# Kernel optimization log

Measured on AMD Instinct MI355X. Metric: run time of the kernel, lower is better.

The kernel has to match this reference:

```python
import jax, jax.numpy as jnp
import numpy as np

N = 32768      # total nodes
E = 524288     # edges (avg degree 16)
HID = 256      # hidden_dim
H = 8          # heads
C = HID // H   # head dim = 32
G = 64         # graphs in batch
NPG = N // G   # nodes per graph = 512
EDIM = 2       # edge feature dim
NEG_SLOPE = 0.2  # PyG GATv2 default


def setup_inputs():
    key = jax.random.key(0)
    ks = jax.random.split(key, 12)
    s = 0.05
    return dict(
        x=jax.random.normal(ks[0], (N, HID), jnp.float32),
        edge_attr=jax.random.normal(ks[1], (E, EDIM), jnp.float32),
        # GATv2Conv params
        W_l=jax.random.normal(ks[2], (HID, HID), jnp.float32) * s,
        b_l=jnp.zeros((HID,), jnp.float32),
        W_r=jax.random.normal(ks[3], (HID, HID), jnp.float32) * s,
        b_r=jnp.zeros((HID,), jnp.float32),
        W_e=jax.random.normal(ks[4], (EDIM, HID), jnp.float32) * s,
        att=jax.random.normal(ks[5], (H, C), jnp.float32) * s,
        bias_gat=jnp.zeros((HID,), jnp.float32),
        # MultiheadAttention params (torch packed qkv layout)
        in_proj_w=jax.random.normal(ks[6], (3 * HID, HID), jnp.float32) * s,
        in_proj_b=jnp.zeros((3 * HID,), jnp.float32),
        out_proj_w=jax.random.normal(ks[7], (HID, HID), jnp.float32) * s,
        out_proj_b=jnp.zeros((HID,), jnp.float32),
        alpha_param=jnp.array(0.5, jnp.float32),
        # FFN
        W1=jax.random.normal(ks[8], (HID, 4 * HID), jnp.float32) * s,
        b1=jnp.zeros((4 * HID,), jnp.float32),
        W2=jax.random.normal(ks[9], (4 * HID, HID), jnp.float32) * s,
        b2=jnp.zeros((HID,), jnp.float32),
        # LayerNorms
        g1=jnp.ones((HID,), jnp.float32), be1=jnp.zeros((HID,), jnp.float32),
        g2=jnp.ones((HID,), jnp.float32), be2=jnp.zeros((HID,), jnp.float32),
        g3=jnp.ones((HID,), jnp.float32), be3=jnp.zeros((HID,), jnp.float32),
        edge_index=jax.random.randint(ks[10], (2, E), 0, N, jnp.int32),
        batch=jnp.repeat(jnp.arange(G, dtype=jnp.int32), NPG),
    )


def _ln(x, g, b, eps=1e-5):
    m = jnp.mean(x, -1, keepdims=True)
    v = jnp.mean((x - m) ** 2, -1, keepdims=True)
    return (x - m) * jax.lax.rsqrt(v + eps) * g + b


def _gatv2(x, edge_index, edge_attr, W_l, b_l, W_r, b_r, W_e, att, bias_gat):
    src, dst = edge_index[0], edge_index[1]
    # PyG add_self_loops with fill_value='mean': self-loop edge_attr at node i
    # is the mean of edge_attr over edges incoming to i (0 if none).
    deg = jax.ops.segment_sum(jnp.ones((E,), x.dtype), dst, num_segments=N)
    ea_mean = jax.ops.segment_sum(edge_attr, dst, num_segments=N) / jnp.maximum(deg, 1.0)[:, None]
    loop = jnp.arange(N, dtype=src.dtype)
    src2 = jnp.concatenate([src, loop])
    dst2 = jnp.concatenate([dst, loop])
    ea2 = jnp.concatenate([edge_attr, ea_mean], axis=0)  # [E+N, 2]
    xl = (x @ W_l + b_l).reshape(N, H, C)  # source transform (messages)
    xr = (x @ W_r + b_r).reshape(N, H, C)  # target transform
    ee = (ea2 @ W_e).reshape(-1, H, C)
    e = jax.nn.leaky_relu(xl[src2] + xr[dst2] + ee, NEG_SLOPE)  # [E+N, H, C]
    score = jnp.einsum('ehc,hc->eh', e, att)  # [E+N, H]
    # scatter softmax over incoming edges of each target node
    smax = jax.lax.stop_gradient(jax.ops.segment_max(score, dst2, num_segments=N))
    ex = jnp.exp(score - smax[dst2])
    ssum = jax.ops.segment_sum(ex, dst2, num_segments=N)
    alpha = ex / ssum[dst2]  # [E+N, H]
    out = jax.ops.segment_sum(alpha[:, :, None] * xl[src2], dst2, num_segments=N)
    return out.reshape(N, HID) + bias_gat


def _mha(xg, in_proj_w, in_proj_b, out_proj_w, out_proj_b):
    # xg: [G, NPG, HID]; torch nn.MultiheadAttention (batch_first, eval mode)
    qkv = xg @ in_proj_w.T + in_proj_b
    q, k, v = jnp.split(qkv, 3, axis=-1)
    q = q.reshape(G, NPG, H, C)
    k = k.reshape(G, NPG, H, C)
    v = v.reshape(G, NPG, H, C)
    scores = jnp.einsum('gqhd,gkhd->ghqk', q, k) / jnp.sqrt(jnp.float32(C))
    p = jax.nn.softmax(scores, axis=-1)
    o = jnp.einsum('ghqk,gkhd->gqhd', p, v).reshape(G, NPG, HID)
    return o @ out_proj_w.T + out_proj_b


def reference(x, edge_attr, W_l, b_l, W_r, b_r, W_e, att, bias_gat,
              in_proj_w, in_proj_b, out_proj_w, out_proj_b, alpha_param,
              W1, b1, W2, b2, g1, be1, g2, be2, g3, be3, edge_index, batch):
    local_out = _ln(
        _gatv2(x, edge_index, edge_attr, W_l, b_l, W_r, b_r, W_e, att, bias_gat),
        g1, be1)
    # batch is sorted with equal-sized graphs -> the per-graph ragged
    # attention loop equals one batched [G, NPG, NPG] attention
    xg = x.reshape(G, NPG, HID)
    global_out = _mha(xg, in_proj_w, in_proj_b, out_proj_w, out_proj_b).reshape(N, HID)
    global_out = _ln(global_out, g2, be2)
    a = jax.nn.sigmoid(alpha_param)
    combined = a * local_out + (1.0 - a) * global_out
    ffn = jax.nn.gelu(combined @ W1 + b1, approximate=False) @ W2 + b2
    return _ln(combined + ffn, g3, be3)
```

## Files before the change

### kernel.cpp

```cpp
#include <hip/hip_runtime.h>
#include <math.h>

#define N_NODES 32768
#define E_EDGES 524288
#define HIDDEN  256
#define NPG     512
#define NGRAPH  64
#define NHEAD   8
#define CDIM    32

typedef unsigned short bf16;
typedef __attribute__((ext_vector_type(8))) short short8;
typedef __attribute__((ext_vector_type(4))) float f4;

#define AS1 __attribute__((address_space(1)))
#define AS3 __attribute__((address_space(3)))

__device__ __forceinline__ void cp16(const bf16* g, bf16* l) {
    __builtin_amdgcn_global_load_lds((AS1 const unsigned int*)(const void*)g,
                                     (AS3 unsigned int*)(void*)l, 16, 0, 0);
}

__device__ inline float bf2f(unsigned short u) {
    union { unsigned int i; float f; } v; v.i = ((unsigned int)u) << 16; return v.f;
}
__device__ inline unsigned short f2bf(float f) {
    union { float f; unsigned int i; } v; v.f = f;
    unsigned int x = v.i;
    return (unsigned short)((x + 0x7FFFu + ((x >> 16) & 1u)) >> 16);
}
__device__ inline float4 load4(const float* p) { return *(const float4*)p; }
__device__ inline float4 load4(const bf16* p) {
    ushort4 u = *(const ushort4*)p;
    return make_float4(bf2f(u.x), bf2f(u.y), bf2f(u.z), bf2f(u.w));
}
__device__ inline void store4(float* p, float4 v) { *(float4*)p = v; }
__device__ inline void store4(bf16* p, float4 v) {
    ushort4 u; u.x = f2bf(v.x); u.y = f2bf(v.y); u.z = f2bf(v.z); u.w = f2bf(v.w);
    *(ushort4*)p = u;
}


__global__ void zero_kernel(float* deg, float* ea_sum, int* fill) {
    int i = blockIdx.x * blockDim.x + threadIdx.x;
    if (i < 2 * N_NODES) ea_sum[i] = 0.0f;
    if (i < N_NODES) { deg[i] = 0.0f; fill[i] = 0; }
}

__global__ void deg_kernel(const int* __restrict__ ei, const float* __restrict__ edge_attr,
                           float* deg, float* ea_sum) {
    int e = blockIdx.x * blockDim.x + threadIdx.x;
    if (e >= E_EDGES) return;
    int d = ei[E_EDGES + e];
    atomicAdd(&deg[d], 1.0f);
    atomicAdd(&ea_sum[2 * d + 0], edge_attr[2 * e + 0]);
    atomicAdd(&ea_sum[2 * d + 1], edge_attr[2 * e + 1]);
}

__global__ void eamean_kernel(const float* __restrict__ deg, float* ea_mean) {
    int i = blockIdx.x * blockDim.x + threadIdx.x;
    if (i >= N_NODES) return;
    float dm = fmaxf(deg[i], 1.0f);
    ea_mean[2 * i + 0] /= dm;
    ea_mean[2 * i + 1] /= dm;
}

__global__ __launch_bounds__(1024) void scan_kernel(const float* __restrict__ deg, int* row_ptr) {
    __shared__ int part[1024];
    int t = threadIdx.x;
    int base = t * 32;
    int loc[32];
    int s = 0;
    #pragma unroll
    for (int j = 0; j < 32; j++) {
        loc[j] = s;
        s += (int)deg[base + j] + 1;
    }
    int mysum = s;
    part[t] = s;
    __syncthreads();
    for (int off = 1; off < 1024; off <<= 1) {
        int v = 0;
        if (t >= off) v = part[t - off];
        __syncthreads();
        part[t] += v;
        __syncthreads();
    }
    int offset = part[t] - mysum;
    #pragma unroll
    for (int j = 0; j < 32; j++) row_ptr[base + j] = offset + loc[j];
    if (t == 1023) row_ptr[N_NODES] = part[1023];
}

__global__ void fill_kernel(const int* __restrict__ ei, const int* __restrict__ row_ptr,
                            int* fill, int* col) {
    int tid = blockIdx.x * blockDim.x + threadIdx.x;
    if (tid >= E_EDGES + N_NODES) return;
    int d;
    if (tid < E_EDGES) d = ei[E_EDGES + tid];
    else               d = tid - E_EDGES;
    int pos = row_ptr[d] + atomicAdd(&fill[d], 1);
    col[pos] = tid;
}

__global__ void convall(const float* __restrict__ x,
                        const float* __restrict__ W_l, const float* __restrict__ W_r,
                        const float* __restrict__ W1, const float* __restrict__ W2,
                        const float* __restrict__ in_proj_w, const float* __restrict__ out_proj_w,
                        const float* __restrict__ b_l, const float* __restrict__ b_r,
                        bf16* xb, bf16* wlrb, bf16* w1b, bf16* w2b,
                        bf16* wipb, bf16* wopb, float* blr)
{
    int b = blockIdx.x, t = threadIdx.x;
    if (b < 8192) {
        int i = b * 256 + t;
        store4(&xb[i * 4], *(const float4*)&x[i * 4]);
    } else if (b < 8448) {
        int i = (b - 8192) * 256 + t; int k = i >> 8, n = i & 255;
        wlrb[n * 256 + k] = f2bf(W_l[i]);
    } else if (b < 8704) {
        int i = (b - 8448) * 256 + t; int k = i >> 8, n = i & 255;
        wlrb[(256 + n) * 256 + k] = f2bf(W_r[i]);
    } else if (b < 9728) {
        int i = (b - 8704) * 256 + t; int k = i >> 10, n = i & 1023;
        w1b[n * 256 + k] = f2bf(W1[i]);
    } else if (b < 10752) {
        int i = (b - 9728) * 256 + t; int k = i >> 8, n = i & 255;
        w2b[n * 1024 + k] = f2bf(W2[i]);
    } else if (b < 10944) {
        int i = (b - 10752) * 256 + t;
        store4(&wipb[i * 4], *(const float4*)&in_proj_w[i * 4]);
    } else if (b < 11008) {
        int i = (b - 10944) * 256 + t;
        store4(&wopb[i * 4], *(const float4*)&out_proj_w[i * 4]);
    } else {
        blr[t] = b_l[t]; blr[256 + t] = b_r[t];
    }
}

template <int EPI>
__global__ __launch_bounds__(256) void mfma_gemm(
    const bf16* __restrict__ A, const bf16* __restrict__ Wb,
    const float* __restrict__ bias, const bf16* __restrict__ res,
    bf16* __restrict__ C, int M, int N, int K)
{
    __shared__ bf16 lds[2 * 128 * 64];
    bf16* As = lds;
    bf16* Bs = lds + 128 * 64;
    int tid = threadIdx.x;
    int wave = tid >> 6, lane = tid & 63;
    int quad = lane >> 4, l16 = lane & 15;
    int n0 = blockIdx.x * 128, m0 = blockIdx.y * 128;
    int wm = (wave & 1) * 64, wn = (wave >> 1) * 64;

    f4 acc[4][4] = {};

    int srow = tid >> 3;
    int scol = (tid & 7) * 8;

    for (int k0 = 0; k0 < K; k0 += 64) {
        #pragma unroll
        for (int i = 0; i < 4; i++) {
            int row = i * 32 + srow;
            cp16(&A[(size_t)(m0 + row) * K + k0 + scol], &As[row * 64 + scol]);
            cp16(&Wb[(size_t)(n0 + row) * K + k0 + scol], &Bs[row * 64 + scol]);
        }
        __syncthreads();
        #pragma unroll
        for (int ks = 0; ks < 2; ks++) {
            short8 af[4], bfr[4];
            #pragma unroll
            for (int mt = 0; mt < 4; mt++)
                af[mt] = *(const short8*)&As[(wm + mt * 16 + l16) * 64 + ks * 32 + quad * 8];
            #pragma unroll
            for (int nt = 0; nt < 4; nt++)
                bfr[nt] = *(const short8*)&Bs[(wn + nt * 16 + l16) * 64 + ks * 32 + quad * 8];
            #pragma unroll
            for (int mt = 0; mt < 4; mt++)
                #pragma unroll
                for (int nt = 0; nt < 4; nt++)
                    acc[mt][nt] = __builtin_amdgcn_mfma_f32_16x16x32_bf16(
                        af[mt], bfr[nt], acc[mt][nt], 0, 0, 0);
        }
        __syncthreads();
    }

    float* epi = (float*)lds + wave * 16 * 68;
    int row = lane >> 2;
    int cb = (lane & 3) * 16;
    int gn = n0 + wn + cb;
    float bb[16];
    *(float4*)&bb[0]  = *(const float4*)&bias[gn + 0];
    *(float4*)&bb[4]  = *(const float4*)&bias[gn + 4];
    *(float4*)&bb[8]  = *(const float4*)&bias[gn + 8];
    *(float4*)&bb[12] = *(const float4*)&bias[gn + 12];

    for (int mt = 0; mt < 4; mt++) {
        #pragma unroll
        for (int nt = 0; nt < 4; nt++)
            #pragma unroll
            for (int r = 0; r < 4; r++)
                epi[(quad * 4 + r) * 68 + nt * 16 + l16] = acc[mt][nt][r];
        float vv[16];
        *(float4*)&vv[0]  = *(float4*)&epi[row * 68 + cb + 0];
        *(float4*)&vv[4]  = *(float4*)&epi[row * 68 + cb + 4];
        *(float4*)&vv[8]  = *(float4*)&epi[row * 68 + cb + 8];
        *(float4*)&vv[12] = *(float4*)&epi[row * 68 + cb + 12];
        int gm = m0 + wm + mt * 16 + row;
        #pragma unroll
        for (int j = 0; j < 16; j++) vv[j] += bb[j];
        if (EPI == 1) {
            #pragma unroll
            for (int j = 0; j < 16; j++)
                vv[j] = 0.5f * vv[j] * (1.0f + erff(vv[j] * 0.70710678118654752f));
        } else if (EPI == 2) {
            ushort rr[16];
            const bf16* rp = &res[(size_t)gm * N + gn];
            *(int4*)&rr[0] = *(const int4*)&rp[0];
            *(int4*)&rr[8] = *(const int4*)&rp[8];
            #pragma unroll
            for (int j = 0; j < 16; j++) vv[j] += bf2f(rr[j]);
        }
        ushort o16[16];
        #pragma unroll
        for (int j = 0; j < 16; j++) o16[j] = f2bf(vv[j]);
        bf16* cp = &C[(size_t)gm * N + gn];
        *(int4*)&cp[0] = *(int4*)&o16[0];
        *(int4*)&cp[8] = *(int4*)&o16[8];
    }
}

__global__ __launch_bounds__(256) void attn_mfma(
    const bf16* __restrict__ qkv, bf16* __restrict__ attnout)
{
    __shared__ bf16 Ks[128 * 40];
    __shared__ bf16 Vt[32 * 136];
    __shared__ bf16 Pb[4 * 64 * 40];

    int b = blockIdx.x;
    int g = b >> 4, h = (b >> 1) & 7, hlf = b & 1;
    int tid = threadIdx.x;
    int wave = tid >> 6, lane = tid & 63;
    int quad = lane >> 4, l16 = lane & 15;
    int qbase = hlf * 256 + wave * 64;
    bf16* Pw = &Pb[wave * 64 * 40];
    const float SCALE = 0.17677669529663687f;

    short8 qf[4];
    #pragma unroll
    for (int mt = 0; mt < 4; mt++) {
        size_t node = (size_t)(g * NPG + qbase + mt * 16 + l16);
        qf[mt] = *(const short8*)&qkv[node * 768 + h * CDIM + quad * 8];
    }

    f4 oacc[4][2] = {};
    float lacc[4][4] = {};

    for (int c = 0; c < 4; c++) {
        int kk0 = c * 128;
        __syncthreads();
        #pragma unroll
        for (int i = 0; i < 2; i++) {
            int idx = i * 256 + tid;
            int key = idx >> 2, kc = (idx & 3) * 8;
            *(int4*)&Ks[key * 40 + kc] =
                *(const int4*)&qkv[(size_t)(g * NPG + kk0 + key) * 768 + 256 + h * CDIM + kc];
        }
        {
            int key = tid >> 1, dblk = (tid & 1) * 16;
            ushort tmp[16];
            const bf16* vp = &qkv[(size_t)(g * NPG + kk0 + key) * 768 + 512 + h * CDIM + dblk];
            *(int4*)&tmp[0] = *(const int4*)&vp[0];
            *(int4*)&tmp[8] = *(const int4*)&vp[8];
            #pragma unroll
            for (int j = 0; j < 16; j++) Vt[(dblk + j) * 136 + key] = tmp[j];
        }
        __syncthreads();

        for (int sub = 0; sub < 4; sub++) {
            int ks0 = sub * 32;
            short8 kf[2];
            #pragma unroll
            for (int nt = 0; nt < 2; nt++)
                kf[nt] = *(const short8*)&Ks[(ks0 + nt * 16 + l16) * 40 + quad * 8];
            #pragma unroll
            for (int mt = 0; mt < 4; mt++) {
                #pragma unroll
                for (int nt = 0; nt < 2; nt++) {
                    f4 z = {0.f, 0.f, 0.f, 0.f};
                    f4 s = __builtin_amdgcn_mfma_f32_16x16x32_bf16(qf[mt], kf[nt], z, 0, 0, 0);
                    #pragma unroll
                    for (int r = 0; r < 4; r++) {
                        float p = __expf(s[r] * SCALE);
                        lacc[mt][r] += p;
                        Pw[(mt * 16 + quad * 4 + r) * 40 + nt * 16 + l16] = f2bf(p);
                    }
                }
            }
            short8 vf[2];
            #pragma unroll
            for (int dt = 0; dt < 2; dt++)
                vf[dt] = *(const short8*)&Vt[(dt * 16 + l16) * 136 + ks0 + quad * 8];
            #pragma unroll
            for (int mt = 0; mt < 4; mt++) {
                short8 pf = *(const short8*)&Pw[(mt * 16 + l16) * 40 + quad * 8];
                #pragma unroll
                for (int dt = 0; dt < 2; dt++)
                    oacc[mt][dt] = __builtin_amdgcn_mfma_f32_16x16x32_bf16(
                        pf, vf[dt], oacc[mt][dt], 0, 0, 0);
            }
        }
    }

    #pragma unroll
    for (int mt = 0; mt < 4; mt++)
        #pragma unroll
        for (int r = 0; r < 4; r++) {
            float l = lacc[mt][r];
            l += __shfl_xor(l, 1);
            l += __shfl_xor(l, 2);
            l += __shfl_xor(l, 4);
            l += __shfl_xor(l, 8);
            lacc[mt][r] = l;
        }

    #pragma unroll
    for (int mt = 0; mt < 4; mt++) {
        #pragma unroll
        for (int dt = 0; dt < 2; dt++) {
            #pragma unroll
            for (int r = 0; r < 4; r++) {
                float v = oacc[mt][dt][r] / lacc[mt][r];
                size_t node = (size_t)(g * NPG + qbase + mt * 16 + quad * 4 + r);
                attnout[node * HIDDEN + h * CDIM + dt * 16 + l16] = f2bf(v);
            }
        }
    }
}

__device__ __forceinline__ void fetchmeta(
    int i, int re, int node, const int* __restrict__ col, const int* __restrict__ ei,
    const float* __restrict__ edge_attr, const float* __restrict__ ea_mean,
    int& s, float& a0, float& a1)
{
    if (i < re) {
        int e = col[i];
        if (e < E_EDGES) {
            s = ei[e]; a0 = edge_attr[2 * e]; a1 = edge_attr[2 * e + 1];
        } else {
            s = node; a0 = ea_mean[2 * node]; a1 = ea_mean[2 * node + 1];
        }
    } else {
        s = node; a0 = 0.f; a1 = 0.f;
    }
}

__global__ __launch_bounds__(256) void gat_kernel(
    const bf16* __restrict__ xlr,
    const int* __restrict__ row_ptr, const int* __restrict__ col,
    const int* __restrict__ ei, const float* __restrict__ edge_attr,
    const float* __restrict__ ea_mean,
    const float* __restrict__ W_e, const float* __restrict__ att,
    const float* __restrict__ bias_gat,
    const float* __restrict__ g1, const float* __restrict__ be1,
    bf16* __restrict__ out)
{
    __shared__ float pacc[2][260];
    __shared__ float plsum[2][64];
    int wave = threadIdx.x >> 6;
    int lane = threadIdx.x & 63;
    int nloc = wave >> 1, half = wave & 1;
    int node = blockIdx.x * 2 + nloc;
    int cb = lane * 4;

    float4 xr4 = load4(&xlr[(size_t)node * 512 + 256 + cb]);
    float4 we0 = *(const float4*)&W_e[cb];
    float4 we1 = *(const float4*)&W_e[HIDDEN + cb];
    float4 at4 = *(const float4*)&att[cb];

    int rs = row_ptr[node], re = row_ptr[node + 1];

    float lsum = 0.f;
    float acc0 = 0.f, acc1 = 0.f, acc2 = 0.f, acc3 = 0.f;

    int i0 = rs + half;
    int s0, s1; float a00, a01, a10, a11;
    fetchmeta(i0,     re, node, col, ei, edge_attr, ea_mean, s0, a00, a01);
    fetchmeta(i0 + 2, re, node, col, ei, edge_attr, ea_mean, s1, a10, a11);
    ushort4 xu0 = *(const ushort4*)&xlr[(size_t)s0 * 512 + cb];

    for (int i = i0; i < re; i += 2) {
        int s2; float a20, a21;
        fetchmeta(i + 4, re, node, col, ei, edge_attr, ea_mean, s2, a20, a21);
        ushort4 xu1 = *(const ushort4*)&xlr[(size_t)s1 * 512 + cb];

        float4 xl4 = make_float4(bf2f(xu0.x), bf2f(xu0.y), bf2f(xu0.z), bf2f(xu0.w));
        float t, p = 0.f;
        t = xl4.x + xr4.x + a00 * we0.x + a01 * we1.x; t = (t > 0.f) ? t : 0.2f * t; p += t * at4.x;
        t = xl4.y + xr4.y + a00 * we0.y + a01 * we1.y; t = (t > 0.f) ? t : 0.2f * t; p += t * at4.y;
        t = xl4.z + xr4.z + a00 * we0.z + a01 * we1.z; t = (t > 0.f) ? t : 0.2f * t; p += t * at4.z;
        t = xl4.w + xr4.w + a00 * we0.w + a01 * we1.w; t = (t > 0.f) ? t : 0.2f * t; p += t * at4.w;
        p += __shfl_xor(p, 1);
        p += __shfl_xor(p, 2);
        p += __shfl_xor(p, 4);
        float w = __expf(p);
        lsum += w;
        acc0 += w * xl4.x; acc1 += w * xl4.y; acc2 += w * xl4.z; acc3 += w * xl4.w;

        s0 = s1; a00 = a10; a01 = a11; xu0 = xu1;
        s1 = s2; a10 = a20; a11 = a21;
    }

    if (half) {
        plsum[nloc][lane] = lsum;
        pacc[nloc][cb + 0] = acc0; pacc[nloc][cb + 1] = acc1;
        pacc[nloc][cb + 2] = acc2; pacc[nloc][cb + 3] = acc3;
    }
    __syncthreads();
    if (!half) {
        lsum += plsum[nloc][lane];
        acc0 += pacc[nloc][cb + 0]; acc1 += pacc[nloc][cb + 1];
        acc2 += pacc[nloc][cb + 2]; acc3 += pacc[nloc][cb + 3];

        float inv = 1.0f / lsum;
        float v0 = acc0 * inv + bias_gat[cb + 0];
        float v1 = acc1 * inv + bias_gat[cb + 1];
        float v2 = acc2 * inv + bias_gat[cb + 2];
        float v3 = acc3 * inv + bias_gat[cb + 3];

        float s = v0 + v1 + v2 + v3;
        #pragma unroll
        for (int m = 1; m < 64; m <<= 1) s += __shfl_xor(s, m);
        float mean = s * (1.0f / 256.0f);
        float d0 = v0 - mean, d1 = v1 - mean, d2 = v2 - mean, d3 = v3 - mean;
        float sq = d0 * d0 + d1 * d1 + d2 * d2 + d3 * d3;
        #pragma unroll
        for (int m = 1; m < 64; m <<= 1) sq += __shfl_xor(sq, m);
        float rstd = rsqrtf(sq * (1.0f / 256.0f) + 1e-5f);
        float4 o;
        o.x = d0 * rstd * g1[cb + 0] + be1[cb + 0];
        o.y = d1 * rstd * g1[cb + 1] + be1[cb + 1];
        o.z = d2 * rstd * g1[cb + 2] + be1[cb + 2];
        o.w = d3 * rstd * g1[cb + 3] + be1[cb + 3];
        store4(&out[(size_t)node * HIDDEN + cb], o);
    }
}

__global__ __launch_bounds__(256) void combine_kernel(
    const bf16* __restrict__ gout, const bf16* __restrict__ localout,
    const float* __restrict__ alpha_p,
    const float* __restrict__ g2, const float* __restrict__ be2,
    bf16* __restrict__ combined)
{
    int wave = threadIdx.x >> 6;
    int lane = threadIdx.x & 63;
    int node = blockIdx.x * 4 + wave;
    int cb = lane * 4;
    float4 gv = load4(&gout[(size_t)node * HIDDEN + cb]);
    float s = gv.x + gv.y + gv.z + gv.w;
    #pragma unroll
    for (int m = 1; m < 64; m <<= 1) s += __shfl_xor(s, m);
    float mean = s * (1.0f / 256.0f);
    float d0 = gv.x - mean, d1 = gv.y - mean, d2 = gv.z - mean, d3 = gv.w - mean;
    float sq = d0 * d0 + d1 * d1 + d2 * d2 + d3 * d3;
    #pragma unroll
    for (int m = 1; m < 64; m <<= 1) sq += __shfl_xor(sq, m);
    float rstd = rsqrtf(sq * (1.0f / 256.0f) + 1e-5f);
    float n0 = d0 * rstd * g2[cb + 0] + be2[cb + 0];
    float n1 = d1 * rstd * g2[cb + 1] + be2[cb + 1];
    float n2 = d2 * rstd * g2[cb + 2] + be2[cb + 2];
    float n3 = d3 * rstd * g2[cb + 3] + be2[cb + 3];
    float a = 1.0f / (1.0f + __expf(-alpha_p[0]));
    float4 lv = load4(&localout[(size_t)node * HIDDEN + cb]);
    float4 o;
    o.x = a * lv.x + (1.0f - a) * n0;
    o.y = a * lv.y + (1.0f - a) * n1;
    o.z = a * lv.z + (1.0f - a) * n2;
    o.w = a * lv.w + (1.0f - a) * n3;
    store4(&combined[(size_t)node * HIDDEN + cb], o);
}

__global__ __launch_bounds__(256) void finalln_kernel(
    const bf16* __restrict__ ffn,
    const float* __restrict__ g3, const float* __restrict__ be3,
    float* __restrict__ out)
{
    int wave = threadIdx.x >> 6;
    int lane = threadIdx.x & 63;
    int node = blockIdx.x * 4 + wave;
    int cb = lane * 4;
    float4 v = load4(&ffn[(size_t)node * HIDDEN + cb]);
    float s = v.x + v.y + v.z + v.w;
    #pragma unroll
    for (int m = 1; m < 64; m <<= 1) s += __shfl_xor(s, m);
    float mean = s * (1.0f / 256.0f);
    float d0 = v.x - mean, d1 = v.y - mean, d2 = v.z - mean, d3 = v.w - mean;
    float sq = d0 * d0 + d1 * d1 + d2 * d2 + d3 * d3;
    #pragma unroll
    for (int m = 1; m < 64; m <<= 1) sq += __shfl_xor(sq, m);
    float rstd = rsqrtf(sq * (1.0f / 256.0f) + 1e-5f);
    float4 o;
    o.x = d0 * rstd * g3[cb + 0] + be3[cb + 0];
    o.y = d1 * rstd * g3[cb + 1] + be3[cb + 1];
    o.z = d2 * rstd * g3[cb + 2] + be3[cb + 2];
    o.w = d3 * rstd * g3[cb + 3] + be3[cb + 3];
    *(float4*)&out[(size_t)node * HIDDEN + cb] = o;
}

extern "C" void kernel_launch(void* const* d_in, const int* in_sizes, int n_in,
                              void* d_out, int out_size, void* d_ws, size_t ws_size,
                              hipStream_t stream) {
    const float* x          = (const float*)d_in[0];
    const float* edge_attr  = (const float*)d_in[1];
    const float* W_l        = (const float*)d_in[2];
    const float* b_l        = (const float*)d_in[3];
    const float* W_r        = (const float*)d_in[4];
    const float* b_r        = (const float*)d_in[5];
    const float* W_e        = (const float*)d_in[6];
    const float* att        = (const float*)d_in[7];
    const float* bias_gat   = (const float*)d_in[8];
    const float* in_proj_w  = (const float*)d_in[9];
    const float* in_proj_b  = (const float*)d_in[10];
    const float* out_proj_w = (const float*)d_in[11];
    const float* out_proj_b = (const float*)d_in[12];
    const float* alpha_p    = (const float*)d_in[13];
    const float* W1         = (const float*)d_in[14];
    const float* b1         = (const float*)d_in[15];
    const float* W2         = (const float*)d_in[16];
    const float* b2         = (const float*)d_in[17];
    const float* g1  = (const float*)d_in[18];
    const float* be1 = (const float*)d_in[19];
    const float* g2  = (const float*)d_in[20];
    const float* be2 = (const float*)d_in[21];
    const float* g3  = (const float*)d_in[22];
    const float* be3 = (const float*)d_in[23];
    const int* edge_index = (const int*)d_in[24];

    char* base = (char*)d_ws;
    const size_t MB = 1024 * 1024;
    const size_t KB = 1024;
    float* deg     = (float*)(base + 0);
    float* ea_mean = (float*)(base + 131072);
    int*   fill    = (int*)  (base + 393216);
    int*   row_ptr = (int*)  (base + 524288);
    int*   col     = (int*)  (base + 786432);
    bf16* wlrb = (bf16*)(base + 3 * MB);
    bf16* wipb = (bf16*)(base + 3 * MB + 256 * KB);
    bf16* wopb = (bf16*)(base + 3 * MB + 640 * KB);
    bf16* w1b  = (bf16*)(base + 3 * MB + 768 * KB);
    bf16* w2b  = (bf16*)(base + 3 * MB + 1280 * KB);
    float* blr = (float*)(base + 5 * MB);
    bf16* xb       = (bf16*)(base + 8 * MB);
    bf16* qkv      = (bf16*)(base + 24 * MB);
    bf16* attnout  = (bf16*)(base + 72 * MB);
    bf16* gout     = (bf16*)(base + 24 * MB);
    bf16* xlr      = (bf16*)(base + 40 * MB);
    bf16* localout = (bf16*)(base + 72 * MB);
    bf16* combined = (bf16*)(base + 8 * MB);
    bf16* h1h      = (bf16*)(base + 24 * MB);
    bf16* ffn      = (bf16*)(base + 56 * MB);
    float* out = (float*)d_out;

    zero_kernel<<<(2 * N_NODES + 255) / 256, 256, 0, stream>>>(deg, ea_mean, fill);
    deg_kernel<<<E_EDGES / 256, 256, 0, stream>>>(edge_index, edge_attr, deg, ea_mean);
    eamean_kernel<<<N_NODES / 256, 256, 0, stream>>>(deg, ea_mean);
    scan_kernel<<<1, 1024, 0, stream>>>(deg, row_ptr);
    fill_kernel<<<(E_EDGES + N_NODES) / 256, 256, 0, stream>>>(edge_index, row_ptr, fill, col);

    convall<<<11009, 256, 0, stream>>>(x, W_l, W_r, W1, W2, in_proj_w, out_proj_w,
                                       b_l, b_r, xb, wlrb, w1b, w2b, wipb, wopb, blr);

    mfma_gemm<0><<<dim3(6, 256), 256, 0, stream>>>(
        xb, wipb, in_proj_b, (const bf16*)nullptr, qkv, N_NODES, 768, 256);
    attn_mfma<<<NGRAPH * NHEAD * 2, 256, 0, stream>>>(qkv, attnout);
    mfma_gemm<0><<<dim3(2, 256), 256, 0, stream>>>(
        attnout, wopb, out_proj_b, (const bf16*)nullptr, gout, N_NODES, 256, 256);

    mfma_gemm<0><<<dim3(4, 256), 256, 0, stream>>>(
        xb, wlrb, blr, (const bf16*)nullptr, xlr, N_NODES, 512, 256);
    gat_kernel<<<N_NODES / 2, 256, 0, stream>>>(
        xlr, row_ptr, col, edge_index, edge_attr, ea_mean,
        W_e, att, bias_gat, g1, be1, localout);

    combine_kernel<<<N_NODES / 4, 256, 0, stream>>>(
        gout, localout, alpha_p, g2, be2, combined);

    for (int hh = 0; hh < 2; hh++) {
        const bf16* ch = combined + (size_t)hh * 16384 * 256;
        bf16* fh = ffn + (size_t)hh * 16384 * 256;
        mfma_gemm<1><<<dim3(8, 128), 256, 0, stream>>>(
            ch, w1b, b1, (const bf16*)nullptr, h1h, 16384, 1024, 256);
        mfma_gemm<2><<<dim3(2, 128), 256, 0, stream>>>(
            h1h, w2b, b2, ch, fh, 16384, 256, 1024);
    }

    finalln_kernel<<<N_NODES / 4, 256, 0, stream>>>(ffn, g3, be3, out);
}
```

Baseline: 609.6 us.

## Split GAT xl/xr outputs into dense arrays and transpose attention score MFMA

The x_l/x_r projection GEMM gets a new epilogue that writes its two halves into separate 256-wide arrays, so the GAT gather reads dense 512-byte rows instead of strided halves of 1024-byte rows. In the attention kernel, V is now staged row-major with vector copies instead of a scalar transpose into shared memory. Scores are computed as K·Qᵀ so each lane packs four probabilities into one 8-byte store and accumulates row sums that need only two cross-lane shuffles. The cost is that V fragments are now gathered element by element from shared memory, and the row sums pass through an extra shared buffer.

Measured after the change: 616.3 us. About the same (+1.1%).

```diff
diff --git a/kernel.cpp b/kernel.cpp
--- a/kernel.cpp
+++ b/kernel.cpp
@@ -224,7 +224,14 @@
         ushort o16[16];
         #pragma unroll
         for (int j = 0; j < 16; j++) o16[j] = f2bf(vv[j]);
-        bf16* cp = &C[(size_t)gm * N + gn];
+        bf16* cp;
+        if (EPI == 3) {
+            bf16* dst = (gn < 256) ? C : (bf16*)res;
+            int goff = (gn < 256) ? gn : gn - 256;
+            cp = &dst[(size_t)gm * 256 + goff];
+        } else {
+            cp = &C[(size_t)gm * N + gn];
+        }
         *(int4*)&cp[0] = *(int4*)&o16[0];
         *(int4*)&cp[8] = *(int4*)&o16[8];
     }
@@ -234,8 +241,9 @@
     const bf16* __restrict__ qkv, bf16* __restrict__ attnout)
 {
     __shared__ bf16 Ks[128 * 40];
-    __shared__ bf16 Vt[32 * 136];
+    __shared__ bf16 Vs[128 * 40];
     __shared__ bf16 Pb[4 * 64 * 40];
+    __shared__ float lsumS[4][64];
 
     int b = blockIdx.x;
     int g = b >> 4, h = (b >> 1) & 7, hlf = b & 1;
@@ -248,13 +256,13 @@
 
     short8 qf[4];
     #pragma unroll
-    for (int mt = 0; mt < 4; mt++) {
-        size_t node = (size_t)(g * NPG + qbase + mt * 16 + l16);
-        qf[mt] = *(const short8*)&qkv[node * 768 + h * CDIM + quad * 8];
+    for (int qt = 0; qt < 4; qt++) {
+        size_t node = (size_t)(g * NPG + qbase + qt * 16 + l16);
+        qf[qt] = *(const short8*)&qkv[node * 768 + h * CDIM + quad * 8];
     }
 
     f4 oacc[4][2] = {};
-    float lacc[4][4] = {};
+    float ls[4] = {0.f, 0.f, 0.f, 0.f};
 
     for (int c = 0; c < 4; c++) {
         int kk0 = c * 128;
@@ -263,17 +271,9 @@
         for (int i = 0; i < 2; i++) {
             int idx = i * 256 + tid;
             int key = idx >> 2, kc = (idx & 3) * 8;
-            *(int4*)&Ks[key * 40 + kc] =
-                *(const int4*)&qkv[(size_t)(g * NPG + kk0 + key) * 768 + 256 + h * CDIM + kc];
-        }
-        {
-            int key = tid >> 1, dblk = (tid & 1) * 16;
-            ushort tmp[16];
-            const bf16* vp = &qkv[(size_t)(g * NPG + kk0 + key) * 768 + 512 + h * CDIM + dblk];
-            *(int4*)&tmp[0] = *(const int4*)&vp[0];
-            *(int4*)&tmp[8] = *(const int4*)&vp[8];
-            #pragma unroll
-            for (int j = 0; j < 16; j++) Vt[(dblk + j) * 136 + key] = tmp[j];
+            const bf16* bp = &qkv[(size_t)(g * NPG + kk0 + key) * 768 + h * CDIM + kc];
+            *(int4*)&Ks[key * 40 + kc] = *(const int4*)(bp + 256);
+            *(int4*)&Vs[key * 40 + kc] = *(const int4*)(bp + 512);
         }
         __syncthreads();
 
@@ -281,26 +281,35 @@
             int ks0 = sub * 32;
             short8 kf[2];
             #pragma unroll
-            for (int nt = 0; nt < 2; nt++)
-                kf[nt] = *(const short8*)&Ks[(ks0 + nt * 16 + l16) * 40 + quad * 8];
-            #pragma unroll
-            for (int mt = 0; mt < 4; mt++) {
+            for (int kt = 0; kt < 2; kt++)
+                kf[kt] = *(const short8*)&Ks[(ks0 + kt * 16 + l16) * 40 + quad * 8];
+            #pragma unroll
+            for (int kt = 0; kt < 2; kt++) {
                 #pragma unroll
-                for (int nt = 0; nt < 2; nt++) {
+                for (int qt = 0; qt < 4; qt++) {
                     f4 z = {0.f, 0.f, 0.f, 0.f};
-                    f4 s = __builtin_amdgcn_mfma_f32_16x16x32_bf16(qf[mt], kf[nt], z, 0, 0, 0);
+                    f4 st = __builtin_amdgcn_mfma_f32_16x16x32_bf16(kf[kt], qf[qt], z, 0, 0, 0);
+                    ushort pk[4];
+                    float s4 = 0.f;
                     #pragma unroll
                     for (int r = 0; r < 4; r++) {
-                        float p = __expf(s[r] * SCALE);
-                        lacc[mt][r] += p;
-                        Pw[(mt * 16 + quad * 4 + r) * 40 + nt * 16 + l16] = f2bf(p);
+                        float p = __expf(st[r] * SCALE);
+                        s4 += p;
+                        pk[r] = f2bf(p);
                     }
+                    ls[qt] += s4;
+                    *(uint2*)&Pw[(qt * 16 + l16) * 40 + kt * 16 + quad * 4] = *(uint2*)pk;
                 }
             }
             short8 vf[2];
             #pragma unroll
-            for (int dt = 0; dt < 2; dt++)
-                vf[dt] = *(const short8*)&Vt[(dt * 16 + l16) * 136 + ks0 + quad * 8];
+            for (int dt = 0; dt < 2; dt++) {
+                ushort vtmp[8];
+                #pragma unroll
+                for (int j = 0; j < 8; j++)
+                    vtmp[j] = Vs[(ks0 + quad * 8 + j) * 40 + dt * 16 + l16];
+                vf[dt] = *(short8*)vtmp;
+            }
             #pragma unroll
             for (int mt = 0; mt < 4; mt++) {
                 short8 pf = *(const short8*)&Pw[(mt * 16 + l16) * 40 + quad * 8];
@@ -313,16 +322,13 @@
     }
 
     #pragma unroll
-    for (int mt = 0; mt < 4; mt++)
-        #pragma unroll
-        for (int r = 0; r < 4; r++) {
-            float l = lacc[mt][r];
-            l += __shfl_xor(l, 1);
-            l += __shfl_xor(l, 2);
-            l += __shfl_xor(l, 4);
-            l += __shfl_xor(l, 8);
-            lacc[mt][r] = l;
-        }
+    for (int qt = 0; qt < 4; qt++) {
+        float l = ls[qt];
+        l += __shfl_xor(l, 16);
+        l += __shfl_xor(l, 32);
+        if (quad == 0) lsumS[wave][qt * 16 + l16] = l;
+    }
+    __builtin_amdgcn_s_waitcnt(0);
 
     #pragma unroll
     for (int mt = 0; mt < 4; mt++) {
@@ -330,7 +336,8 @@
         for (int dt = 0; dt < 2; dt++) {
             #pragma unroll
             for (int r = 0; r < 4; r++) {
-                float v = oacc[mt][dt][r] / lacc[mt][r];
+                float denom = lsumS[wave][mt * 16 + quad * 4 + r];
+                float v = oacc[mt][dt][r] / denom;
                 size_t node = (size_t)(g * NPG + qbase + mt * 16 + quad * 4 + r);
                 attnout[node * HIDDEN + h * CDIM + dt * 16 + l16] = f2bf(v);
             }
@@ -356,7 +363,7 @@
 }
 
 __global__ __launch_bounds__(256) void gat_kernel(
-    const bf16* __restrict__ xlr,
+    const bf16* __restrict__ xl, const bf16* __restrict__ xr,
     const int* __restrict__ row_ptr, const int* __restrict__ col,
     const int* __restrict__ ei, const float* __restrict__ edge_attr,
     const float* __restrict__ ea_mean,
@@ -373,7 +380,7 @@
     int node = blockIdx.x * 2 + nloc;
     int cb = lane * 4;
 
-    float4 xr4 = load4(&xlr[(size_t)node * 512 + 256 + cb]);
+    float4 xr4 = load4(&xr[(size_t)node * 256 + cb]);
     float4 we0 = *(const float4*)&W_e[cb];
     float4 we1 = *(const float4*)&W_e[HIDDEN + cb];
     float4 at4 = *(const float4*)&att[cb];
@@ -387,12 +394,12 @@
     int s0, s1; float a00, a01, a10, a11;
     fetchmeta(i0,     re, node, col, ei, edge_attr, ea_mean, s0, a00, a01);
     fetchmeta(i0 + 2, re, node, col, ei, edge_attr, ea_mean, s1, a10, a11);
-    ushort4 xu0 = *(const ushort4*)&xlr[(size_t)s0 * 512 + cb];
+    ushort4 xu0 = *(const ushort4*)&xl[(size_t)s0 * 256 + cb];
 
     for (int i = i0; i < re; i += 2) {
         int s2; float a20, a21;
         fetchmeta(i + 4, re, node, col, ei, edge_attr, ea_mean, s2, a20, a21);
-        ushort4 xu1 = *(const ushort4*)&xlr[(size_t)s1 * 512 + cb];
+        ushort4 xu1 = *(const ushort4*)&xl[(size_t)s1 * 256 + cb];
 
         float4 xl4 = make_float4(bf2f(xu0.x), bf2f(xu0.y), bf2f(xu0.z), bf2f(xu0.w));
         float t, p = 0.f;
@@ -554,7 +561,8 @@
     bf16* qkv      = (bf16*)(base + 24 * MB);
     bf16* attnout  = (bf16*)(base + 72 * MB);
     bf16* gout     = (bf16*)(base + 24 * MB);
-    bf16* xlr      = (bf16*)(base + 40 * MB);
+    bf16* xl       = (bf16*)(base + 40 * MB);
+    bf16* xr       = (bf16*)(base + 56 * MB);
     bf16* localout = (bf16*)(base + 72 * MB);
     bf16* combined = (bf16*)(base + 8 * MB);
     bf16* h1h      = (bf16*)(base + 24 * MB);
@@ -576,10 +584,10 @@
     mfma_gemm<0><<<dim3(2, 256), 256, 0, stream>>>(
         attnout, wopb, out_proj_b, (const bf16*)nullptr, gout, N_NODES, 256, 256);
 
-    mfma_gemm<0><<<dim3(4, 256), 256, 0, stream>>>(
-        xb, wlrb, blr, (const bf16*)nullptr, xlr, N_NODES, 512, 256);
+    mfma_gemm<3><<<dim3(4, 256), 256, 0, stream>>>(
+        xb, wlrb, blr, (const bf16*)xr, xl, N_NODES, 512, 256);
     gat_kernel<<<N_NODES / 2, 256, 0, stream>>>(
-        xlr, row_ptr, col, edge_index, edge_attr, ea_mean,
+        xl, xr, row_ptr, col, edge_index, edge_attr, ea_mean,
         W_e, att, bias_gat, g1, be1, localout);
 
     combine_kernel<<<N_NODES / 4, 256, 0, stream>>>(
```

## Pack CSR edge records and split xl/xr outputs for GAT gather

Applied to the files above, without the earlier changes.

The fill kernel now writes a packed 16-byte record per CSR slot holding the source node and both edge attributes. This replaces the col index that forced gat_kernel to make a dependent second gather into edge_index and edge_attr. The lin_l/lin_r GEMM gets a new epilogue (EPI 3) that writes xl and xr into two separate N x 256 arrays instead of one interleaved 512-wide buffer. Source-row gathers therefore hit a compact array with better cache density. The cost is a larger CSR buffer (16 bytes per edge instead of 4) plus extra reads in fill_kernel.

New measurement: 590.7 us. 3.1% less time.

```diff
diff --git a/kernel.cpp b/kernel.cpp
--- a/kernel.cpp
+++ b/kernel.cpp
@@ -92,15 +92,30 @@
     if (t == 1023) row_ptr[N_NODES] = part[1023];
 }
 
-__global__ void fill_kernel(const int* __restrict__ ei, const int* __restrict__ row_ptr,
-                            int* fill, int* col) {
+__global__ void fill_kernel(const int* __restrict__ ei, const float* __restrict__ edge_attr,
+                            const float* __restrict__ ea_mean,
+                            const int* __restrict__ row_ptr, int* fill, int4* __restrict__ erec) {
     int tid = blockIdx.x * blockDim.x + threadIdx.x;
     if (tid >= E_EDGES + N_NODES) return;
-    int d;
-    if (tid < E_EDGES) d = ei[E_EDGES + tid];
-    else               d = tid - E_EDGES;
+    int d, src; float a0, a1;
+    if (tid < E_EDGES) {
+        d = ei[E_EDGES + tid];
+        src = ei[tid];
+        a0 = edge_attr[2 * tid + 0];
+        a1 = edge_attr[2 * tid + 1];
+    } else {
+        d = tid - E_EDGES;
+        src = d;
+        a0 = ea_mean[2 * d + 0];
+        a1 = ea_mean[2 * d + 1];
+    }
     int pos = row_ptr[d] + atomicAdd(&fill[d], 1);
-    col[pos] = tid;
+    int4 r;
+    r.x = src;
+    r.y = __float_as_int(a0);
+    r.z = __float_as_int(a1);
+    r.w = 0;
+    erec[pos] = r;
 }
 
 __global__ void convall(const float* __restrict__ x,
@@ -224,7 +239,14 @@
         ushort o16[16];
         #pragma unroll
         for (int j = 0; j < 16; j++) o16[j] = f2bf(vv[j]);
-        bf16* cp = &C[(size_t)gm * N + gn];
+        bf16* cp;
+        if (EPI == 3) {
+            bf16* dst = (gn < 256) ? C : (bf16*)res;
+            int goff = (gn < 256) ? gn : gn - 256;
+            cp = &dst[(size_t)gm * 256 + goff];
+        } else {
+            cp = &C[(size_t)gm * N + gn];
+        }
         *(int4*)&cp[0] = *(int4*)&o16[0];
         *(int4*)&cp[8] = *(int4*)&o16[8];
     }
@@ -338,28 +360,21 @@
     }
 }
 
-__device__ __forceinline__ void fetchmeta(
-    int i, int re, int node, const int* __restrict__ col, const int* __restrict__ ei,
-    const float* __restrict__ edge_attr, const float* __restrict__ ea_mean,
+__device__ __forceinline__ void fetchrec(
+    int i, int re, int node, const int4* __restrict__ erec,
     int& s, float& a0, float& a1)
 {
     if (i < re) {
-        int e = col[i];
-        if (e < E_EDGES) {
-            s = ei[e]; a0 = edge_attr[2 * e]; a1 = edge_attr[2 * e + 1];
-        } else {
-            s = node; a0 = ea_mean[2 * node]; a1 = ea_mean[2 * node + 1];
-        }
+        int4 r = erec[i];
+        s = r.x; a0 = __int_as_float(r.y); a1 = __int_as_float(r.z);
     } else {
         s = node; a0 = 0.f; a1 = 0.f;
     }
 }
 
 __global__ __launch_bounds__(256) void gat_kernel(
-    const bf16* __restrict__ xlr,
-    const int* __restrict__ row_ptr, const int* __restrict__ col,
-    const int* __restrict__ ei, const float* __restrict__ edge_attr,
-    const float* __restrict__ ea_mean,
+    const bf16* __restrict__ xl, const bf16* __restrict__ xr,
+    const int* __restrict__ row_ptr, const int4* __restrict__ erec,
     const float* __restrict__ W_e, const float* __restrict__ att,
     const float* __restrict__ bias_gat,
     const float* __restrict__ g1, const float* __restrict__ be1,
@@ -373,7 +388,7 @@
     int node = blockIdx.x * 2 + nloc;
     int cb = lane * 4;
 
-    float4 xr4 = load4(&xlr[(size_t)node * 512 + 256 + cb]);
+    float4 xr4 = load4(&xr[(size_t)node * 256 + cb]);
     float4 we0 = *(const float4*)&W_e[cb];
     float4 we1 = *(const float4*)&W_e[HIDDEN + cb];
     float4 at4 = *(const float4*)&att[cb];
@@ -385,14 +400,14 @@
 
     int i0 = rs + half;
     int s0, s1; float a00, a01, a10, a11;
-    fetchmeta(i0,     re, node, col, ei, edge_attr, ea_mean, s0, a00, a01);
-    fetchmeta(i0 + 2, re, node, col, ei, edge_attr, ea_mean, s1, a10, a11);
-    ushort4 xu0 = *(const ushort4*)&xlr[(size_t)s0 * 512 + cb];
+    fetchrec(i0,     re, node, erec, s0, a00, a01);
+    fetchrec(i0 + 2, re, node, erec, s1, a10, a11);
+    ushort4 xu0 = *(const ushort4*)&xl[(size_t)s0 * 256 + cb];
 
     for (int i = i0; i < re; i += 2) {
         int s2; float a20, a21;
-        fetchmeta(i + 4, re, node, col, ei, edge_attr, ea_mean, s2, a20, a21);
-        ushort4 xu1 = *(const ushort4*)&xlr[(size_t)s1 * 512 + cb];
+        fetchrec(i + 4, re, node, erec, s2, a20, a21);
+        ushort4 xu1 = *(const ushort4*)&xl[(size_t)s1 * 256 + cb];
 
         float4 xl4 = make_float4(bf2f(xu0.x), bf2f(xu0.y), bf2f(xu0.z), bf2f(xu0.w));
         float t, p = 0.f;
@@ -543,7 +558,6 @@
     float* ea_mean = (float*)(base + 131072);
     int*   fill    = (int*)  (base + 393216);
     int*   row_ptr = (int*)  (base + 524288);
-    int*   col     = (int*)  (base + 786432);
     bf16* wlrb = (bf16*)(base + 3 * MB);
     bf16* wipb = (bf16*)(base + 3 * MB + 256 * KB);
     bf16* wopb = (bf16*)(base + 3 * MB + 640 * KB);
@@ -554,18 +568,21 @@
     bf16* qkv      = (bf16*)(base + 24 * MB);
     bf16* attnout  = (bf16*)(base + 72 * MB);
     bf16* gout     = (bf16*)(base + 24 * MB);
-    bf16* xlr      = (bf16*)(base + 40 * MB);
+    bf16* xl       = (bf16*)(base + 40 * MB);
+    bf16* xr       = (bf16*)(base + 56 * MB);
     bf16* localout = (bf16*)(base + 72 * MB);
     bf16* combined = (bf16*)(base + 8 * MB);
     bf16* h1h      = (bf16*)(base + 24 * MB);
     bf16* ffn      = (bf16*)(base + 56 * MB);
+    int4* erec     = (int4*)(base + 88 * MB);
     float* out = (float*)d_out;
 
     zero_kernel<<<(2 * N_NODES + 255) / 256, 256, 0, stream>>>(deg, ea_mean, fill);
     deg_kernel<<<E_EDGES / 256, 256, 0, stream>>>(edge_index, edge_attr, deg, ea_mean);
     eamean_kernel<<<N_NODES / 256, 256, 0, stream>>>(deg, ea_mean);
     scan_kernel<<<1, 1024, 0, stream>>>(deg, row_ptr);
-    fill_kernel<<<(E_EDGES + N_NODES) / 256, 256, 0, stream>>>(edge_index, row_ptr, fill, col);
+    fill_kernel<<<(E_EDGES + N_NODES + 255) / 256, 256, 0, stream>>>(
+        edge_index, edge_attr, ea_mean, row_ptr, fill, erec);
 
     convall<<<11009, 256, 0, stream>>>(x, W_l, W_r, W1, W2, in_proj_w, out_proj_w,
                                        b_l, b_r, xb, wlrb, w1b, w2b, wipb, wopb, blr);
@@ -576,11 +593,10 @@
     mfma_gemm<0><<<dim3(2, 256), 256, 0, stream>>>(
         attnout, wopb, out_proj_b, (const bf16*)nullptr, gout, N_NODES, 256, 256);
 
-    mfma_gemm<0><<<dim3(4, 256), 256, 0, stream>>>(
-        xb, wlrb, blr, (const bf16*)nullptr, xlr, N_NODES, 512, 256);
+    mfma_gemm<3><<<dim3(4, 256), 256, 0, stream>>>(
+        xb, wlrb, blr, (const bf16*)xr, xl, N_NODES, 512, 256);
     gat_kernel<<<N_NODES / 2, 256, 0, stream>>>(
-        xlr, row_ptr, col, edge_index, edge_attr, ea_mean,
-        W_e, att, bias_gat, g1, be1, localout);
+        xl, xr, row_ptr, erec, W_e, att, bias_gat, g1, be1, localout);
 
     combine_kernel<<<N_NODES / 4, 256, 0, stream>>>(
         gout, localout, alpha_p, g2, be2, combined);
```
